# Kernel tuning notes

Hardware: AMD Instinct MI355X
Metric: run time of the kernel (lower is better)

Reference implementation:

```python
import jax, jax.numpy as jnp
import numpy as np

NEG_INF = -jnp.inf


def setup_inputs() -> dict:
    key = jax.random.key(0)
    ks = jax.random.split(key, 8)
    B, Lq, Lk, D, H = 8, 2048, 2048, 256, 128
    queries = jax.random.normal(ks[0], (B, Lq, D), dtype=jnp.float32)
    keys = jax.random.normal(ks[1], (B, Lk, D), dtype=jnp.float32)
    values_1 = jax.random.normal(ks[2], (B, Lk, D), dtype=jnp.float32)
    values_2 = jax.random.normal(ks[3], (B, Lq, D), dtype=jnp.float32)
    values_1_mask = jax.random.randint(ks[4], (B, Lk), 0, 2).astype(bool)
    values_2_mask = jax.random.randint(ks[5], (B, Lq), 0, 2).astype(bool)
    # xavier_normal for Linear(D -> H): std = sqrt(2/(D+H))
    std = float(np.sqrt(2.0 / (D + H)))
    Wq = jax.random.normal(ks[6], (H, D), dtype=jnp.float32) * std
    Wk = jax.random.normal(ks[7], (H, D), dtype=jnp.float32) * std
    scaling = jnp.ones((1, H), dtype=jnp.float32)
    return {
        "queries": queries, "keys": keys,
        "values_1": values_1, "values_1_mask": values_1_mask,
        "values_2": values_2, "values_2_mask": values_2_mask,
        "Wq": Wq, "Wk": Wk, "scaling": scaling,
    }


def reference(queries, keys, values_1, values_1_mask, values_2, values_2_mask, Wq, Wk, scaling):
    # projections + relu (eval mode: dropout inactive)
    pq = jax.nn.relu(jnp.einsum("bqd,hd->bqh", queries, Wq))        # [B,Lq,H]
    pk = jax.nn.relu(jnp.einsum("bkd,hd->bkh", keys, Wk)) * scaling  # [B,Lk,H]
    scores = jnp.einsum("bqh,bkh->bqk", pq, pk)                      # [B,Lq,Lk]

    # branch 2: softmax over queries axis of scores^T, masked by values_2_mask [B,Lq]
    scores_T = jnp.where(values_2_mask[:, None, :], NEG_INF, jnp.swapaxes(scores, 1, 2))  # [B,Lk,Lq]
    alpha_2 = jax.nn.softmax(scores_T, axis=2)
    output_2 = jnp.einsum("bkq,bqd->bkd", alpha_2, values_2)         # [B,Lk,D]

    # branch 1: softmax over keys axis, masked by values_1_mask [B,Lk]
    scores_1 = jnp.where(values_1_mask[:, None, :], NEG_INF, scores)  # [B,Lq,Lk]
    alpha_1 = jax.nn.softmax(scores_1, axis=2)
    output = jnp.einsum("bqk,bkd->bqd", alpha_1, values_1)           # [B,Lq,D]

    return (output, output_2)
```

## Files before the change

### kernel.cpp

```cpp
#include <hip/hip_runtime.h>
#include <cstdint>
#include <math.h>

#define B 8
#define L 2048
#define D 256
#define H 128

typedef __attribute__((ext_vector_type(8))) _Float16 half8;
typedef __attribute__((ext_vector_type(4))) _Float16 half4t;
typedef __attribute__((ext_vector_type(4))) float f32x4;
typedef unsigned short ushort;
typedef unsigned int uint;


__global__ void prep_kernel(const void* __restrict__ raw0,
                            const void* __restrict__ raw1,
                            const float* __restrict__ Wq,
                            const float* __restrict__ Wk,
                            float* __restrict__ fb1,
                            float* __restrict__ fb2,
                            _Float16* __restrict__ Wf) {
    const int t = threadIdx.x;
    const int z = blockIdx.y;
    {
        const void* raw = z ? raw1 : raw0;
        float* outb = z ? fb2 : fb1;
        const uint* wd = (const uint*)raw;
        __shared__ int flag;
        if (t == 0) flag = 0;
        __syncthreads();
        if (wd[t] > 1u) flag = 1;
        __syncthreads();
        const int base = blockIdx.x * 1024;
        if (flag) {
            const uint8_t* by = (const uint8_t*)raw;
#pragma unroll
            for (int j = 0; j < 4; ++j) {
                int i = base + t + 256 * j;
                outb[i] = by[i] ? -INFINITY : 0.f;
            }
        } else {
#pragma unroll
            for (int j = 0; j < 4; ++j) {
                int i = base + t + 256 * j;
                outb[i] = wd[i] ? -INFINITY : 0.f;
            }
        }
    }
    {
        const float* Wsrc = z ? Wk : Wq;
        const int chunk = blockIdx.x * 256 + t;
        const int h = chunk >> 5;
        const int d0 = (chunk & 31) * 8;
        float4 v0 = *(const float4*)(Wsrc + (size_t)h * 256 + d0);
        float4 v1 = *(const float4*)(Wsrc + (size_t)h * 256 + d0 + 4);
        half8 hv;
        hv[0] = (_Float16)v0.x; hv[1] = (_Float16)v0.y;
        hv[2] = (_Float16)v0.z; hv[3] = (_Float16)v0.w;
        hv[4] = (_Float16)v1.x; hv[5] = (_Float16)v1.y;
        hv[6] = (_Float16)v1.z; hv[7] = (_Float16)v1.w;
        const int db = d0 >> 5, dq = (d0 >> 3) & 3;
        size_t off = (size_t)z * 32768 +
                     ((size_t)((h >> 4) * 8 + db)) * 512 + dq * 128 + (h & 15) * 8;
        *(half8*)(Wf + off) = hv;
    }
}

__launch_bounds__(256, 2)
__global__ void proj_mfma_kernel(const float* __restrict__ queries,
                                 const float* __restrict__ keys,
                                 const _Float16* __restrict__ Wf,
                                 const float* __restrict__ scaling,
                                 _Float16* __restrict__ pqo,
                                 _Float16* __restrict__ pko) {
    const int t = threadIdx.x;
    const int w = t >> 6;
    const int lane = t & 63;
    const int l15 = lane & 15;
    const int quad = lane >> 4;
    const int z = blockIdx.z;
    const int half = blockIdx.y;
    const int r0 = blockIdx.x * 64;
    const float* in = z ? keys : queries;
    _Float16* outp = z ? pko : pqo;

    __shared__ __attribute__((aligned(16))) _Float16 Wl[32 * 512];
    __shared__ __attribute__((aligned(16))) _Float16 Af[4][8 * 512];

    {
        const _Float16* wsrc = Wf + ((size_t)z * 64 + half * 32) * 512;
#pragma unroll
        for (int i = 0; i < 8; ++i) {
            const int f = w * 8 + i;
            __builtin_amdgcn_global_load_lds(
                (const __attribute__((address_space(1))) uint*)(wsrc + f * 512 + lane * 8),
                (__attribute__((address_space(3))) uint*)(Wl + f * 512 + lane * 8),
                16, 0, 0);
        }
    }
    {
#pragma unroll
        for (int j = 0; j < 16; ++j) {
            const int idx = t + 256 * j;
            const int row = idx >> 6;
            const int c4 = idx & 63;
            float4 v = *(const float4*)(in + ((size_t)(r0 + row)) * 256 + c4 * 4);
            half4t h4;
            h4[0] = (_Float16)v.x; h4[1] = (_Float16)v.y;
            h4[2] = (_Float16)v.z; h4[3] = (_Float16)v.w;
            const int rt = row >> 4, rl = row & 15;
            const int d0 = c4 * 4;
            const int db = d0 >> 5, dq = (d0 >> 3) & 3, e = d0 & 7;
            *(half4t*)(&Af[rt][db * 512 + dq * 128 + rl * 8 + e]) = h4;
        }
    }
    __syncthreads();

    half8 a[8];
#pragma unroll
    for (int db = 0; db < 8; ++db)
        a[db] = *(const half8*)(&Af[w][db * 512 + lane * 8]);

    f32x4 acc[4];
#pragma unroll
    for (int hti = 0; hti < 4; ++hti) acc[hti] = (f32x4){0.f, 0.f, 0.f, 0.f};
#pragma unroll
    for (int db = 0; db < 8; ++db)
#pragma unroll
        for (int hti = 0; hti < 4; ++hti) {
            half8 bfrag = *(const half8*)(Wl + (hti * 8 + db) * 512 + lane * 8);
            acc[hti] = __builtin_amdgcn_mfma_f32_16x16x32_f16(a[db], bfrag, acc[hti], 0, 0, 0);
        }

    _Float16* S = Af[w];
#pragma unroll
    for (int hti = 0; hti < 4; ++hti) {
        const int hl_ = hti * 16 + l15;
        const int hb = hl_ >> 5, hq = (hl_ >> 3) & 3, e = hl_ & 7;
        const float scl = z ? scaling[half * 64 + hl_] : 1.f;
#pragma unroll
        for (int r = 0; r < 4; ++r) {
            float v = fmaxf(acc[hti][r], 0.f) * scl;
            S[hb * 512 + hq * 128 + (quad * 4 + r) * 8 + e] = (_Float16)v;
        }
    }
    const size_t grow16 = (size_t)(r0 >> 4) + w;
    _Float16* gout = outp + (grow16 * 4 + half * 2) * 512;
#pragma unroll
    for (int hb = 0; hb < 2; ++hb) {
        half8 vv = *(const half8*)(S + hb * 512 + lane * 8);
        *(half8*)(gout + hb * 512 + lane * 8) = vv;
    }
}

__global__ void vtrans_kernel(const float* __restrict__ v1,
                              const float* __restrict__ v2,
                              _Float16* __restrict__ vt1,
                              _Float16* __restrict__ vt2) {
    const int t = threadIdx.x;
    const int zz = blockIdx.z;
    const int b = zz & 7;
    const int which = zz >> 3;
    const float* src = (which ? v2 : v1) + (size_t)b * L * D;
    _Float16* dst = which ? vt2 : vt1;
    const int k0 = blockIdx.x * 64;
    const int d0 = blockIdx.y * 64;
    __shared__ float lt[64][65];
#pragma unroll
    for (int p = 0; p < 4; ++p) {
        int kr = p * 16 + (t >> 4);
        float4 v = *(const float4*)(src + (size_t)(k0 + kr) * D + d0 + (t & 15) * 4);
        lt[(t & 15) * 4 + 0][kr] = v.x;
        lt[(t & 15) * 4 + 1][kr] = v.y;
        lt[(t & 15) * 4 + 2][kr] = v.z;
        lt[(t & 15) * 4 + 3][kr] = v.w;
    }
    __syncthreads();
    const int d = t & 63;
    const int kk = (t >> 6) & 1;
    const int qp = t >> 7;
    const size_t tile = ((size_t)b * L + k0) / 32 + kk;
    const int ct = (d0 + d) >> 4;
    _Float16* base = dst + (tile * 16 + ct) * 512 + (d & 15) * 8;
#pragma unroll
    for (int s = 0; s < 2; ++s) {
        const int qv = qp * 2 + s;
        const float* lr = &lt[d][kk * 32 + qv * 8];
        half8 hv;
#pragma unroll
        for (int e = 0; e < 8; ++e) hv[e] = (_Float16)lr[e];
        *(half8*)(base + qv * 128) = hv;
    }
}

__launch_bounds__(256)
__global__ void score_kernel(const _Float16* __restrict__ pq,
                             const _Float16* __restrict__ pk,
                             const float* __restrict__ fb1,
                             const float* __restrict__ fb2,
                             _Float16* __restrict__ Sb,
                             float* __restrict__ tmax1,
                             float* __restrict__ tmax2,
                             float* __restrict__ mmax) {
    const int t = threadIdx.x;
    const int w = t >> 6;
    const int lane = t & 63;
    const int l15 = lane & 15;
    const int quad = lane >> 4;
    const int bb = blockIdx.z;
    const int k0 = blockIdx.x * 64;
    const int q0 = blockIdx.y * 64;
    const size_t bL = (size_t)bb * L;
    const int qt16 = (q0 >> 4) + w;

    half8 aq[4];
    {
        const _Float16* qb = pq + ((bL + q0 + w * 16) >> 4) * 2048 + lane * 8;
#pragma unroll
        for (int hb = 0; hb < 4; ++hb) aq[hb] = *(const half8*)(qb + hb * 512);
    }

    f32x4 s[4];
#pragma unroll
    for (int jt = 0; jt < 4; ++jt) {
        const _Float16* kb = pk + ((bL + k0 + jt * 16) >> 4) * 2048 + lane * 8;
        f32x4 sv = (f32x4){0.f, 0.f, 0.f, 0.f};
#pragma unroll
        for (int hb = 0; hb < 4; ++hb) {
            half8 bk = *(const half8*)(kb + hb * 512);
            sv = __builtin_amdgcn_mfma_f32_16x16x32_f16(aq[hb], bk, sv, 0, 0, 0);
        }
        s[jt] = sv;
    }

    float b1j[4];
#pragma unroll
    for (int jt = 0; jt < 4; ++jt) b1j[jt] = fb1[bL + k0 + jt * 16 + l15];
    float4 b2v = *(const float4*)(fb2 + bL + q0 + w * 16 + quad * 4);
    float b2r[4] = {b2v.x, b2v.y, b2v.z, b2v.w};

#pragma unroll
    for (int r = 0; r < 4; ++r) {
        float m1 = -INFINITY;
#pragma unroll
        for (int jt = 0; jt < 4; ++jt) m1 = fmaxf(m1, s[jt][r] + b1j[jt]);
        m1 = fmaxf(m1, __shfl_xor(m1, 1));
        m1 = fmaxf(m1, __shfl_xor(m1, 2));
        m1 = fmaxf(m1, __shfl_xor(m1, 4));
        m1 = fmaxf(m1, __shfl_xor(m1, 8));
        if (l15 == 0)
            tmax1[(bL + q0 + w * 16 + quad * 4 + r) * 32 + blockIdx.x] = m1;
    }

#pragma unroll
    for (int jt = 0; jt < 4; ++jt) {
        float m2 = -INFINITY, mm = -INFINITY;
#pragma unroll
        for (int r = 0; r < 4; ++r) {
            m2 = fmaxf(m2, s[jt][r] + b2r[r]);
            mm = fmaxf(mm, s[jt][r]);
        }
        m2 = fmaxf(m2, __shfl_xor(m2, 16));
        m2 = fmaxf(m2, __shfl_xor(m2, 32));
        if (quad == 0)
            tmax2[(bL + k0 + jt * 16 + l15) * 128 + qt16] = m2;
        mm = fmaxf(mm, __shfl_xor(mm, 1));
        mm = fmaxf(mm, __shfl_xor(mm, 2));
        mm = fmaxf(mm, __shfl_xor(mm, 4));
        mm = fmaxf(mm, __shfl_xor(mm, 8));
        mm = fmaxf(mm, __shfl_xor(mm, 16));
        mm = fmaxf(mm, __shfl_xor(mm, 32));
        const size_t mti = ((size_t)bb * 128 + qt16) * 128 + (k0 >> 4) + jt;
        if (lane == 0) mmax[mti] = mm;
        _Float16* sp = Sb + mti * 256 + l15;
#pragma unroll
        for (int r = 0; r < 4; ++r)
            sp[(quad * 4 + r) * 16] = (_Float16)(s[jt][r] - mm);
    }
}

__launch_bounds__(256, 2)
__global__ void attn_pv_kernel(const _Float16* __restrict__ Sb,
                               const float* __restrict__ fb1,
                               const float* __restrict__ fb2,
                               const float* __restrict__ tmax1,
                               const float* __restrict__ tmax2,
                               const float* __restrict__ mmax,
                               const _Float16* __restrict__ vt1,
                               const _Float16* __restrict__ vt2,
                               float* __restrict__ out) {
    const int t = threadIdx.x;
    const int w = t >> 6;
    const int lane = t & 63;
    const int l15 = lane & 15;
    const int quad = lane >> 4;
    const int bb = blockIdx.y;
    const int z = blockIdx.z;
    const int r0 = blockIdx.x * 64;
    const size_t bL = (size_t)bb * L;
    const int qtw = (r0 >> 4) + w;

    const _Float16* Vp = z ? vt2 : vt1;
    const float* fbb = (z ? fb2 : fb1) + bL;
    float* O = out + (z ? (size_t)B * L * D : 0);

    __shared__ __attribute__((aligned(16))) _Float16 kv[2][32 * 512];
    __shared__ __attribute__((aligned(16))) _Float16 sst[2][4096];

    auto stage = [&](int it, int buf) {
        const _Float16* vb = Vp + ((bL + (size_t)it * 64) >> 5) * (size_t)(16 * 512);
#pragma unroll
        for (int i = 0; i < 8; ++i) {
            const int c = w * 8 + i;
            __builtin_amdgcn_global_load_lds(
                (const __attribute__((address_space(1))) uint*)(vb + c * 512 + lane * 8),
                (__attribute__((address_space(3))) uint*)(&kv[buf][c * 512] + lane * 8),
                16, 0, 0);
        }
#pragma unroll
        for (int j = 0; j < 2; ++j) {
            const _Float16* ssrc;
            if (z == 0) {
                ssrc = Sb + (((size_t)bb * 128 + qtw) * 128 + it * 4) * 256 +
                       j * 512 + lane * 8;
            } else {
                const int qt = it * 4 + j * 2 + (lane >> 5);
                ssrc = Sb + (((size_t)bb * 128 + qt) * 128 + qtw) * 256 +
                       (lane & 31) * 8;
            }
            __builtin_amdgcn_global_load_lds(
                (const __attribute__((address_space(1))) uint*)ssrc,
                (__attribute__((address_space(3))) uint*)(&sst[buf][w * 1024 + j * 512] + lane * 8),
                16, 0, 0);
        }
    };

    stage(0, 0);

    float mreg;
    {
        const int row = r0 + w * 16 + l15;
        float mv = -INFINITY;
        if (z == 0) {
            const float4* p4 = (const float4*)(tmax1 + ((bL + row) << 5)) + quad * 2;
#pragma unroll
            for (int i = 0; i < 2; ++i) {
                float4 v = p4[i];
                mv = fmaxf(mv, fmaxf(fmaxf(v.x, v.y), fmaxf(v.z, v.w)));
            }
        } else {
            const float4* p4 = (const float4*)(tmax2 + ((bL + row) << 7)) + quad * 8;
#pragma unroll
            for (int i = 0; i < 8; ++i) {
                float4 v = p4[i];
                mv = fmaxf(mv, fmaxf(fmaxf(v.x, v.y), fmaxf(v.z, v.w)));
            }
        }
        mv = fmaxf(mv, __shfl_xor(mv, 16));
        mv = fmaxf(mv, __shfl_xor(mv, 32));
        mreg = fmaxf(mv, -1e30f);
    }

    stage(1, 1);

    asm volatile("s_waitcnt vmcnt(10)" ::: "memory");
    __builtin_amdgcn_sched_barrier(0);
    __builtin_amdgcn_s_barrier();
    __builtin_amdgcn_sched_barrier(0);

    f32x4 acc[16];
#pragma unroll
    for (int ct = 0; ct < 16; ++ct) acc[ct] = (f32x4){0.f, 0.f, 0.f, 0.f};
    float lsum = 0.f;

    for (int it = 0; it < 32; ++it) {
        const int buf = it & 1;
#pragma unroll
        for (int jt2 = 0; jt2 < 2; ++jt2) {
            const int mt = jt2 * 2 + (quad >> 1);
            float c;
            if (z == 0)
                c = mmax[((size_t)bb * 128 + qtw) * 128 + it * 4 + mt] - mreg;
            else
                c = mmax[((size_t)bb * 128 + it * 4 + mt) * 128 + qtw] - mreg;
            float bj[8];
            {
                const float4* bp = (const float4*)(fbb + it * 64 + jt2 * 32 + quad * 8);
                float4 b0 = bp[0], b1 = bp[1];
                bj[0] = b0.x; bj[1] = b0.y; bj[2] = b0.z; bj[3] = b0.w;
                bj[4] = b1.x; bj[5] = b1.y; bj[6] = b1.z; bj[7] = b1.w;
            }
            float pj[8];
            if (z == 0) {
                const _Float16* sl =
                    &sst[buf][w * 1024 + mt * 256 + l15 * 16 + (quad & 1) * 8];
                half8 sv = *(const half8*)sl;
#pragma unroll
                for (int j = 0; j < 8; ++j) pj[j] = (float)sv[j];
            } else {
                const _Float16* sl = &sst[buf][w * 1024 + mt * 256 + l15];
#pragma unroll
                for (int j = 0; j < 8; ++j)
                    pj[j] = (float)sl[((quad & 1) * 8 + j) * 16];
            }
            half8 pa;
#pragma unroll
            for (int j = 0; j < 8; ++j) {
                float p = __expf(pj[j] + c + bj[j]);
                pa[j] = (_Float16)p;
                lsum += (float)pa[j];
            }
            const _Float16* kb = &kv[buf][jt2 * 16 * 512];
#pragma unroll
            for (int ct = 0; ct < 16; ++ct) {
                half8 bv = *(const half8*)(kb + ct * 512 + lane * 8);
                acc[ct] = __builtin_amdgcn_mfma_f32_16x16x32_f16(pa, bv, acc[ct], 0, 0, 0);
            }
        }

        if (it < 31) {
            __builtin_amdgcn_s_barrier();
            __builtin_amdgcn_sched_barrier(0);
            if (it + 2 < 32) {
                stage(it + 2, buf);
                asm volatile("s_waitcnt vmcnt(10)" ::: "memory");
            } else {
                asm volatile("s_waitcnt vmcnt(0)" ::: "memory");
            }
            __builtin_amdgcn_sched_barrier(0);
            __builtin_amdgcn_s_barrier();
            __builtin_amdgcn_sched_barrier(0);
        }
    }

    lsum += __shfl_xor(lsum, 16);
    lsum += __shfl_xor(lsum, 32);
    float inv = (lsum > 0.f) ? (1.f / lsum) : 0.f;

#pragma unroll
    for (int r = 0; r < 4; ++r) {
        const float invr = __shfl(inv, quad * 4 + r);
        float* orow = O + (bL + r0 + w * 16 + quad * 4 + r) * (size_t)D + l15;
#pragma unroll
        for (int ct = 0; ct < 16; ++ct)
            orow[ct * 16] = acc[ct][r] * invr;
    }
}

extern "C" void kernel_launch(void* const* d_in, const int* in_sizes, int n_in,
                              void* d_out, int out_size, void* d_ws, size_t ws_size,
                              hipStream_t stream) {
    const float* queries  = (const float*)d_in[0];
    const float* keys     = (const float*)d_in[1];
    const float* values_1 = (const float*)d_in[2];
    const void*  v1_mask  = d_in[3];
    const float* values_2 = (const float*)d_in[4];
    const void*  v2_mask  = d_in[5];
    const float* Wq       = (const float*)d_in[6];
    const float* Wk       = (const float*)d_in[7];
    const float* scaling  = (const float*)d_in[8];
    float* out = (float*)d_out;

    _Float16* pqw = (_Float16*)d_ws;
    _Float16* pkw = pqw + (size_t)B * L * H;
    _Float16* vt1 = pkw + (size_t)B * L * H;
    _Float16* vt2 = vt1 + (size_t)B * L * D;
    _Float16* Sb  = vt2 + (size_t)B * L * D;
    float* fb1   = (float*)(Sb + (size_t)B * 128 * 128 * 256);
    float* fb2   = fb1 + B * L;
    float* tmax1 = fb2 + B * L;
    float* tmax2 = tmax1 + (size_t)B * L * 32;
    float* mmaxp = tmax2 + (size_t)B * L * 128;
    _Float16* Wf = (_Float16*)(mmaxp + (size_t)B * 128 * 128);

    prep_kernel<<<dim3(16, 2), 256, 0, stream>>>(
        v1_mask, v2_mask, Wq, Wk, fb1, fb2, Wf);
    proj_mfma_kernel<<<dim3(B * L / 64, 2, 2), 256, 0, stream>>>(
        queries, keys, Wf, scaling, pqw, pkw);
    vtrans_kernel<<<dim3(L / 64, D / 64, B * 2), 256, 0, stream>>>(
        values_1, values_2, vt1, vt2);
    score_kernel<<<dim3(L / 64, L / 64, B), 256, 0, stream>>>(
        pqw, pkw, fb1, fb2, Sb, tmax1, tmax2, mmaxp);
    attn_pv_kernel<<<dim3(L / 64, B, 2), 256, 0, stream>>>(
        Sb, fb1, fb2, tmax1, tmax2, mmaxp, vt1, vt2, out);
}
```

Before: 247.5 us.

## Fuse score computation into attention kernel with online softmax

Drops the separate score kernel, which wrote a half-precision score matrix and per-tile maxima to global memory. The fused kernel now recomputes QK^T per 32-key tile from the projected Q/K held in LDS, using the flash-attention style online softmax. Rescaling is lazy and happens only when the tile max rises more than 8 above the running max. This removes the large score round-trip through memory and one launch. In exchange it repeats the QK MFMAs for each branch (K and Q are swapped for branch 2), adds an LDS round-trip to transpose P, and lets values exceed 1 before the fp16 conversion.

```diff
diff --git a/kernel.cpp b/kernel.cpp
--- a/kernel.cpp
+++ b/kernel.cpp
@@ -9,6 +9,7 @@
 
 typedef __attribute__((ext_vector_type(8))) _Float16 half8;
 typedef __attribute__((ext_vector_type(4))) _Float16 half4t;
+typedef __attribute__((ext_vector_type(2))) _Float16 half2v;
 typedef __attribute__((ext_vector_type(4))) float f32x4;
 typedef unsigned short ushort;
 typedef unsigned int uint;
@@ -194,102 +195,14 @@
     }
 }
 
-__launch_bounds__(256)
-__global__ void score_kernel(const _Float16* __restrict__ pq,
-                             const _Float16* __restrict__ pk,
-                             const float* __restrict__ fb1,
-                             const float* __restrict__ fb2,
-                             _Float16* __restrict__ Sb,
-                             float* __restrict__ tmax1,
-                             float* __restrict__ tmax2,
-                             float* __restrict__ mmax) {
-    const int t = threadIdx.x;
-    const int w = t >> 6;
-    const int lane = t & 63;
-    const int l15 = lane & 15;
-    const int quad = lane >> 4;
-    const int bb = blockIdx.z;
-    const int k0 = blockIdx.x * 64;
-    const int q0 = blockIdx.y * 64;
-    const size_t bL = (size_t)bb * L;
-    const int qt16 = (q0 >> 4) + w;
-
-    half8 aq[4];
-    {
-        const _Float16* qb = pq + ((bL + q0 + w * 16) >> 4) * 2048 + lane * 8;
-#pragma unroll
-        for (int hb = 0; hb < 4; ++hb) aq[hb] = *(const half8*)(qb + hb * 512);
-    }
-
-    f32x4 s[4];
-#pragma unroll
-    for (int jt = 0; jt < 4; ++jt) {
-        const _Float16* kb = pk + ((bL + k0 + jt * 16) >> 4) * 2048 + lane * 8;
-        f32x4 sv = (f32x4){0.f, 0.f, 0.f, 0.f};
-#pragma unroll
-        for (int hb = 0; hb < 4; ++hb) {
-            half8 bk = *(const half8*)(kb + hb * 512);
-            sv = __builtin_amdgcn_mfma_f32_16x16x32_f16(aq[hb], bk, sv, 0, 0, 0);
-        }
-        s[jt] = sv;
-    }
-
-    float b1j[4];
-#pragma unroll
-    for (int jt = 0; jt < 4; ++jt) b1j[jt] = fb1[bL + k0 + jt * 16 + l15];
-    float4 b2v = *(const float4*)(fb2 + bL + q0 + w * 16 + quad * 4);
-    float b2r[4] = {b2v.x, b2v.y, b2v.z, b2v.w};
-
-#pragma unroll
-    for (int r = 0; r < 4; ++r) {
-        float m1 = -INFINITY;
-#pragma unroll
-        for (int jt = 0; jt < 4; ++jt) m1 = fmaxf(m1, s[jt][r] + b1j[jt]);
-        m1 = fmaxf(m1, __shfl_xor(m1, 1));
-        m1 = fmaxf(m1, __shfl_xor(m1, 2));
-        m1 = fmaxf(m1, __shfl_xor(m1, 4));
-        m1 = fmaxf(m1, __shfl_xor(m1, 8));
-        if (l15 == 0)
-            tmax1[(bL + q0 + w * 16 + quad * 4 + r) * 32 + blockIdx.x] = m1;
-    }
-
-#pragma unroll
-    for (int jt = 0; jt < 4; ++jt) {
-        float m2 = -INFINITY, mm = -INFINITY;
-#pragma unroll
-        for (int r = 0; r < 4; ++r) {
-            m2 = fmaxf(m2, s[jt][r] + b2r[r]);
-            mm = fmaxf(mm, s[jt][r]);
-        }
-        m2 = fmaxf(m2, __shfl_xor(m2, 16));
-        m2 = fmaxf(m2, __shfl_xor(m2, 32));
-        if (quad == 0)
-            tmax2[(bL + k0 + jt * 16 + l15) * 128 + qt16] = m2;
-        mm = fmaxf(mm, __shfl_xor(mm, 1));
-        mm = fmaxf(mm, __shfl_xor(mm, 2));
-        mm = fmaxf(mm, __shfl_xor(mm, 4));
-        mm = fmaxf(mm, __shfl_xor(mm, 8));
-        mm = fmaxf(mm, __shfl_xor(mm, 16));
-        mm = fmaxf(mm, __shfl_xor(mm, 32));
-        const size_t mti = ((size_t)bb * 128 + qt16) * 128 + (k0 >> 4) + jt;
-        if (lane == 0) mmax[mti] = mm;
-        _Float16* sp = Sb + mti * 256 + l15;
-#pragma unroll
-        for (int r = 0; r < 4; ++r)
-            sp[(quad * 4 + r) * 16] = (_Float16)(s[jt][r] - mm);
-    }
-}
-
 __launch_bounds__(256, 2)
-__global__ void attn_pv_kernel(const _Float16* __restrict__ Sb,
-                               const float* __restrict__ fb1,
-                               const float* __restrict__ fb2,
-                               const float* __restrict__ tmax1,
-                               const float* __restrict__ tmax2,
-                               const float* __restrict__ mmax,
-                               const _Float16* __restrict__ vt1,
-                               const _Float16* __restrict__ vt2,
-                               float* __restrict__ out) {
+__global__ void attn_fused_kernel(const _Float16* __restrict__ pqw,
+                                  const _Float16* __restrict__ pkw,
+                                  const float* __restrict__ fb1,
+                                  const float* __restrict__ fb2,
+                                  const _Float16* __restrict__ vt1,
+                                  const _Float16* __restrict__ vt2,
+                                  float* __restrict__ out) {
     const int t = threadIdx.x;
     const int w = t >> 6;
     const int lane = t & 63;
@@ -299,72 +212,51 @@
     const int z = blockIdx.z;
     const int r0 = blockIdx.x * 64;
     const size_t bL = (size_t)bb * L;
-    const int qtw = (r0 >> 4) + w;
-
+
+    const _Float16* Qp = z ? pkw : pqw;
+    const _Float16* Kp = z ? pqw : pkw;
     const _Float16* Vp = z ? vt2 : vt1;
     const float* fbb = (z ? fb2 : fb1) + bL;
     float* O = out + (z ? (size_t)B * L * D : 0);
 
-    __shared__ __attribute__((aligned(16))) _Float16 kv[2][32 * 512];
-    __shared__ __attribute__((aligned(16))) _Float16 sst[2][4096];
+    __shared__ __attribute__((aligned(16))) _Float16 klds[2][4096];
+    __shared__ __attribute__((aligned(16))) _Float16 vlds[2][8192];
+    __shared__ __attribute__((aligned(16))) _Float16 plds[4][512];
 
     auto stage = [&](int it, int buf) {
-        const _Float16* vb = Vp + ((bL + (size_t)it * 64) >> 5) * (size_t)(16 * 512);
-#pragma unroll
-        for (int i = 0; i < 8; ++i) {
-            const int c = w * 8 + i;
+        const _Float16* ksrc = Kp + ((bL + it * 32) >> 4) * 2048;
+#pragma unroll
+        for (int i = 0; i < 2; ++i) {
+            const int c = w * 2 + i;
             __builtin_amdgcn_global_load_lds(
-                (const __attribute__((address_space(1))) uint*)(vb + c * 512 + lane * 8),
-                (__attribute__((address_space(3))) uint*)(&kv[buf][c * 512] + lane * 8),
+                (const __attribute__((address_space(1))) uint*)(ksrc + c * 512 + lane * 8),
+                (__attribute__((address_space(3))) uint*)(&klds[buf][c * 512] + lane * 8),
                 16, 0, 0);
         }
-#pragma unroll
-        for (int j = 0; j < 2; ++j) {
-            const _Float16* ssrc;
-            if (z == 0) {
-                ssrc = Sb + (((size_t)bb * 128 + qtw) * 128 + it * 4) * 256 +
-                       j * 512 + lane * 8;
-            } else {
-                const int qt = it * 4 + j * 2 + (lane >> 5);
-                ssrc = Sb + (((size_t)bb * 128 + qt) * 128 + qtw) * 256 +
-                       (lane & 31) * 8;
-            }
+        const _Float16* vsrc = Vp + ((bL + it * 32) >> 5) * (size_t)8192;
+#pragma unroll
+        for (int i = 0; i < 4; ++i) {
+            const int c = w * 4 + i;
             __builtin_amdgcn_global_load_lds(
-                (const __attribute__((address_space(1))) uint*)ssrc,
-                (__attribute__((address_space(3))) uint*)(&sst[buf][w * 1024 + j * 512] + lane * 8),
+                (const __attribute__((address_space(1))) uint*)(vsrc + c * 512 + lane * 8),
+                (__attribute__((address_space(3))) uint*)(&vlds[buf][c * 512] + lane * 8),
                 16, 0, 0);
         }
     };
 
+    half8 aq[4];
+    {
+        const _Float16* qb = Qp + ((bL + r0 + w * 16) >> 4) * 2048 + lane * 8;
+#pragma unroll
+        for (int hb = 0; hb < 4; ++hb) aq[hb] = *(const half8*)(qb + hb * 512);
+    }
+
     stage(0, 0);
-
-    float mreg;
-    {
-        const int row = r0 + w * 16 + l15;
-        float mv = -INFINITY;
-        if (z == 0) {
-            const float4* p4 = (const float4*)(tmax1 + ((bL + row) << 5)) + quad * 2;
-#pragma unroll
-            for (int i = 0; i < 2; ++i) {
-                float4 v = p4[i];
-                mv = fmaxf(mv, fmaxf(fmaxf(v.x, v.y), fmaxf(v.z, v.w)));
-            }
-        } else {
-            const float4* p4 = (const float4*)(tmax2 + ((bL + row) << 7)) + quad * 8;
-#pragma unroll
-            for (int i = 0; i < 8; ++i) {
-                float4 v = p4[i];
-                mv = fmaxf(mv, fmaxf(fmaxf(v.x, v.y), fmaxf(v.z, v.w)));
-            }
-        }
-        mv = fmaxf(mv, __shfl_xor(mv, 16));
-        mv = fmaxf(mv, __shfl_xor(mv, 32));
-        mreg = fmaxf(mv, -1e30f);
-    }
-
+    float4 bc0 = *(const float4*)(fbb + quad * 4);
+    float4 bc1 = *(const float4*)(fbb + 16 + quad * 4);
     stage(1, 1);
 
-    asm volatile("s_waitcnt vmcnt(10)" ::: "memory");
+    asm volatile("s_waitcnt vmcnt(6)" ::: "memory");
     __builtin_amdgcn_sched_barrier(0);
     __builtin_amdgcn_s_barrier();
     __builtin_amdgcn_sched_barrier(0);
@@ -373,58 +265,84 @@
 #pragma unroll
     for (int ct = 0; ct < 16; ++ct) acc[ct] = (f32x4){0.f, 0.f, 0.f, 0.f};
     float lsum = 0.f;
-
-    for (int it = 0; it < 32; ++it) {
+    float m = -1e30f;
+
+    const int NT = 64;
+#pragma unroll 2
+    for (int it = 0; it < NT; ++it) {
         const int buf = it & 1;
-#pragma unroll
-        for (int jt2 = 0; jt2 < 2; ++jt2) {
-            const int mt = jt2 * 2 + (quad >> 1);
-            float c;
-            if (z == 0)
-                c = mmax[((size_t)bb * 128 + qtw) * 128 + it * 4 + mt] - mreg;
-            else
-                c = mmax[((size_t)bb * 128 + it * 4 + mt) * 128 + qtw] - mreg;
-            float bj[8];
-            {
-                const float4* bp = (const float4*)(fbb + it * 64 + jt2 * 32 + quad * 8);
-                float4 b0 = bp[0], b1 = bp[1];
-                bj[0] = b0.x; bj[1] = b0.y; bj[2] = b0.z; bj[3] = b0.w;
-                bj[4] = b1.x; bj[5] = b1.y; bj[6] = b1.z; bj[7] = b1.w;
-            }
-            float pj[8];
-            if (z == 0) {
-                const _Float16* sl =
-                    &sst[buf][w * 1024 + mt * 256 + l15 * 16 + (quad & 1) * 8];
-                half8 sv = *(const half8*)sl;
-#pragma unroll
-                for (int j = 0; j < 8; ++j) pj[j] = (float)sv[j];
-            } else {
-                const _Float16* sl = &sst[buf][w * 1024 + mt * 256 + l15];
-#pragma unroll
-                for (int j = 0; j < 8; ++j)
-                    pj[j] = (float)sl[((quad & 1) * 8 + j) * 16];
-            }
-            half8 pa;
-#pragma unroll
-            for (int j = 0; j < 8; ++j) {
-                float p = __expf(pj[j] + c + bj[j]);
-                pa[j] = (_Float16)p;
-                lsum += (float)pa[j];
-            }
-            const _Float16* kb = &kv[buf][jt2 * 16 * 512];
-#pragma unroll
-            for (int ct = 0; ct < 16; ++ct) {
-                half8 bv = *(const half8*)(kb + ct * 512 + lane * 8);
-                acc[ct] = __builtin_amdgcn_mfma_f32_16x16x32_f16(pa, bv, acc[ct], 0, 0, 0);
-            }
-        }
-
-        if (it < 31) {
+
+        float4 bn0 = bc0, bn1 = bc1;
+        if (it + 1 < NT) {
+            bn0 = *(const float4*)(fbb + (it + 1) * 32 + quad * 4);
+            bn1 = *(const float4*)(fbb + (it + 1) * 32 + 16 + quad * 4);
+        }
+
+        f32x4 s0 = (f32x4){0.f, 0.f, 0.f, 0.f};
+        f32x4 s1 = (f32x4){0.f, 0.f, 0.f, 0.f};
+#pragma unroll
+        for (int hb = 0; hb < 4; ++hb) {
+            half8 kf0 = *(const half8*)(&klds[buf][hb * 512 + lane * 8]);
+            half8 kf1 = *(const half8*)(&klds[buf][2048 + hb * 512 + lane * 8]);
+            s0 = __builtin_amdgcn_mfma_f32_16x16x32_f16(kf0, aq[hb], s0, 0, 0, 0);
+            s1 = __builtin_amdgcn_mfma_f32_16x16x32_f16(kf1, aq[hb], s1, 0, 0, 0);
+        }
+        float sv0[4], sv1[4];
+        float mt_ = -INFINITY;
+#pragma unroll
+        for (int r = 0; r < 4; ++r) {
+            sv0[r] = s0[r] + ((const float*)&bc0)[r];
+            sv1[r] = s1[r] + ((const float*)&bc1)[r];
+            mt_ = fmaxf(mt_, fmaxf(sv0[r], sv1[r]));
+        }
+        mt_ = fmaxf(mt_, __shfl_xor(mt_, 16));
+        mt_ = fmaxf(mt_, __shfl_xor(mt_, 32));
+
+        if (!__all(mt_ <= m + 8.f)) {
+            float mn = fmaxf(m, mt_);
+            float sc = __expf(m - mn);
+            m = mn;
+            lsum *= sc;
+#pragma unroll
+            for (int ct = 0; ct < 16; ++ct) acc[ct] *= sc;
+        }
+
+        float psum = 0.f;
+        float p0[4], p1[4];
+#pragma unroll
+        for (int r = 0; r < 4; ++r) {
+            p0[r] = __expf(sv0[r] - m);
+            p1[r] = __expf(sv1[r] - m);
+            psum += p0[r] + p1[r];
+        }
+        lsum += psum;
+        half2v q00; q00[0] = (_Float16)p0[0]; q00[1] = (_Float16)p0[1];
+        half2v q01; q01[0] = (_Float16)p0[2]; q01[1] = (_Float16)p0[3];
+        half2v q10; q10[0] = (_Float16)p1[0]; q10[1] = (_Float16)p1[1];
+        half2v q11; q11[0] = (_Float16)p1[2]; q11[1] = (_Float16)p1[3];
+        _Float16* pw = &plds[w][0];
+        const int eb0 = (quad >> 1) * 128 + l15 * 8 + (quad & 1) * 4;
+        const int eb1 = (2 + (quad >> 1)) * 128 + l15 * 8 + (quad & 1) * 4;
+        *(half2v*)(pw + eb0) = q00;
+        *(half2v*)(pw + eb0 + 2) = q01;
+        *(half2v*)(pw + eb1) = q10;
+        *(half2v*)(pw + eb1 + 2) = q11;
+        half8 pfrag = *(const half8*)(pw + lane * 8);
+
+#pragma unroll
+        for (int ct = 0; ct < 16; ++ct) {
+            half8 vf = *(const half8*)(&vlds[buf][ct * 512 + lane * 8]);
+            acc[ct] = __builtin_amdgcn_mfma_f32_16x16x32_f16(vf, pfrag, acc[ct], 0, 0, 0);
+        }
+
+        bc0 = bn0; bc1 = bn1;
+
+        if (it < NT - 1) {
             __builtin_amdgcn_s_barrier();
             __builtin_amdgcn_sched_barrier(0);
-            if (it + 2 < 32) {
+            if (it + 2 < NT) {
                 stage(it + 2, buf);
-                asm volatile("s_waitcnt vmcnt(10)" ::: "memory");
+                asm volatile("s_waitcnt vmcnt(6)" ::: "memory");
             } else {
                 asm volatile("s_waitcnt vmcnt(0)" ::: "memory");
             }
@@ -436,15 +354,14 @@
 
     lsum += __shfl_xor(lsum, 16);
     lsum += __shfl_xor(lsum, 32);
-    float inv = (lsum > 0.f) ? (1.f / lsum) : 0.f;
-
-#pragma unroll
-    for (int r = 0; r < 4; ++r) {
-        const float invr = __shfl(inv, quad * 4 + r);
-        float* orow = O + (bL + r0 + w * 16 + quad * 4 + r) * (size_t)D + l15;
-#pragma unroll
-        for (int ct = 0; ct < 16; ++ct)
-            orow[ct * 16] = acc[ct][r] * invr;
+    const float inv = (lsum > 0.f) ? (1.f / lsum) : 0.f;
+
+    const int qrow = r0 + w * 16 + l15;
+    float* orow = O + (bL + qrow) * (size_t)D + quad * 4;
+#pragma unroll
+    for (int ct = 0; ct < 16; ++ct) {
+        f32x4 v = acc[ct] * inv;
+        *(f32x4*)(orow + ct * 16) = v;
     }
 }
 
@@ -466,13 +383,9 @@
     _Float16* pkw = pqw + (size_t)B * L * H;
     _Float16* vt1 = pkw + (size_t)B * L * H;
     _Float16* vt2 = vt1 + (size_t)B * L * D;
-    _Float16* Sb  = vt2 + (size_t)B * L * D;
-    float* fb1   = (float*)(Sb + (size_t)B * 128 * 128 * 256);
+    float* fb1   = (float*)(vt2 + (size_t)B * L * D);
     float* fb2   = fb1 + B * L;
-    float* tmax1 = fb2 + B * L;
-    float* tmax2 = tmax1 + (size_t)B * L * 32;
-    float* mmaxp = tmax2 + (size_t)B * L * 128;
-    _Float16* Wf = (_Float16*)(mmaxp + (size_t)B * 128 * 128);
+    _Float16* Wf = (_Float16*)(fb2 + B * L);
 
     prep_kernel<<<dim3(16, 2), 256, 0, stream>>>(
         v1_mask, v2_mask, Wq, Wk, fb1, fb2, Wf);
@@ -480,8 +393,6 @@
         queries, keys, Wf, scaling, pqw, pkw);
     vtrans_kernel<<<dim3(L / 64, D / 64, B * 2), 256, 0, stream>>>(
         values_1, values_2, vt1, vt2);
-    score_kernel<<<dim3(L / 64, L / 64, B), 256, 0, stream>>>(
-        pqw, pkw, fb1, fb2, Sb, tmax1, tmax2, mmaxp);
-    attn_pv_kernel<<<dim3(L / 64, B, 2), 256, 0, stream>>>(
-        Sb, fb1, fb2, tmax1, tmax2, mmaxp, vt1, vt2, out);
-}
+    attn_fused_kernel<<<dim3(L / 64, B, 2), 256, 0, stream>>>(
+        pqw, pkw, fb1, fb2, vt1, vt2, out);
+}
```

Result: faster. 227.4 us (-8.1%).
